# Performance work log

Hardware: AMD Instinct MI355X
Metric: run time of the kernel (lower is better)

Reference implementation:

```python
import jax, jax.numpy as jnp
import numpy as np

PZ = 8            # pz half-patch in get_dist_base
P = 2 * PZ        # patch side = 16
C, T, HF, WF = 128, 3, 256, 256
N = 2048          # number of keypoint pairs


def setup_inputs() -> dict:
    key = jax.random.key(0)
    ks = jax.random.split(key, 9)
    response = jax.random.normal(ks[0], (C, T, HF, WF), dtype=jnp.float32)
    ys1 = jax.random.randint(ks[1], (N,), 0, HF - P, dtype=jnp.int32)
    xs1 = jax.random.randint(ks[2], (N,), 0, WF - P, dtype=jnp.int32)
    ts1 = jax.random.randint(ks[3], (N,), 0, T, dtype=jnp.int32)
    ys2 = jax.random.randint(ks[4], (N,), 0, HF - P, dtype=jnp.int32)
    xs2 = jax.random.randint(ks[5], (N,), 0, WF - P, dtype=jnp.int32)
    ts2 = jax.random.randint(ks[6], (N,), 0, T, dtype=jnp.int32)
    pair_type = jax.random.randint(ks[7], (N,), 0, 3, dtype=jnp.int32)  # 0=BG,1=I,2=IS
    powers = 1.0 + jax.random.uniform(ks[8], (3,), dtype=jnp.float32)   # per-type exponent in [1,2)
    plus = jnp.ones((1,), dtype=jnp.float32)
    return dict(response=response, ys1=ys1, xs1=xs1, ts1=ts1,
                ys2=ys2, xs2=xs2, ts2=ts2, pair_type=pair_type,
                powers=powers, plus=plus)


def _gather_patches(response, ts, ys, xs):
    # response: [C, T, Hf, Wf] -> patches [N, C, P, P]
    c = response.shape[0]
    def one(t, y, x):
        return jax.lax.dynamic_slice(response, (0, t, y, x), (c, 1, P, P))[:, 0]
    return jax.vmap(one)(ts, ys, xs)


def _minmax_norm(p):
    # normalize_tensor: min-max over whole patch; identity if max==min
    mn = p.min(axis=(1, 2, 3), keepdims=True)
    mx = p.max(axis=(1, 2, 3), keepdims=True)
    rng = mx - mn
    return jnp.where(rng != 0, (p - mn) / jnp.where(rng == 0, 1.0, rng), p)


def reference(response, ys1, xs1, ts1, ys2, xs2, ts2, pair_type, powers, plus):
    P1 = _minmax_norm(_gather_patches(response, ts1, ys1, xs1))
    P2 = _minmax_norm(_gather_patches(response, ts2, ys2, xs2))
    pw = powers[pair_type][:, None, None, None]            # per-pair exponent
    d = jnp.mean(jnp.abs(P1 - P2) ** pw, axis=(1, 2, 3))   # losscal core, [N]
    per = jnp.where(pair_type == 2, d, 1.0 / (1.0 + d))    # IS -> losscal_1, BG/I -> losscal_2
    per = per + jnp.where(pair_type == 0, 0.0, plus[0] * 0.5)  # + plus/2 for I and IS
    return jnp.mean(per)                                   # lossbase / act
```

## Files before the change

### kernel.cpp

```cpp
#include <hip/hip_runtime.h>
#include <math.h>

#define CC 128
#define TT 3
#define HFD 256
#define WFD 256
#define PP 16
#define NPAIR 2048
#define HW (HFD * WFD)
#define POS (TT * HW)
#define CH_STRIDE POS
#define PATCH_ELEMS (CC * PP * PP)
#define BLOCK 256
#define TP 256

typedef float floatx2 __attribute__((ext_vector_type(2)));
typedef float floatx4 __attribute__((ext_vector_type(4)));

__global__ __launch_bounds__(BLOCK) void transpose_minmax_kernel(
    const float* __restrict__ resp,
    unsigned int* __restrict__ rt32,
    float* __restrict__ cmn, float* __restrict__ cmx) {
    __shared__ unsigned int tile32[TP][33];
    __shared__ float smn[4][TP], smx[4][TP];

    int p0 = blockIdx.x * TP;
    int pc = threadIdx.x & 63;
    int ph = threadIdx.x >> 6;

    const float* bp = resp + p0 + 4 * pc;

    float mn0 = INFINITY, mn1 = INFINITY, mn2 = INFINITY, mn3 = INFINITY;
    float mx0 = -INFINITY, mx1 = -INFINITY, mx2 = -INFINITY, mx3 = -INFINITY;

    #pragma unroll
    for (int k = 0; k < 8; ++k) {
        int q = k * 4 + ph;
        floatx4 l0 = *(const floatx4*)(bp + (size_t)(4 * q + 0) * CH_STRIDE);
        floatx4 l1 = *(const floatx4*)(bp + (size_t)(4 * q + 1) * CH_STRIDE);
        floatx4 l2 = *(const floatx4*)(bp + (size_t)(4 * q + 2) * CH_STRIDE);
        floatx4 l3 = *(const floatx4*)(bp + (size_t)(4 * q + 3) * CH_STRIDE);
        #pragma unroll
        for (int j = 0; j < 4; ++j) {
            float v0 = l0[j], v1 = l1[j], v2 = l2[j], v3 = l3[j];
            float mnj = fminf(fminf(v0, v1), fminf(v2, v3));
            float mxj = fmaxf(fmaxf(v0, v1), fmaxf(v2, v3));
            if (j == 0) { mn0 = fminf(mn0, mnj); mx0 = fmaxf(mx0, mxj); }
            if (j == 1) { mn1 = fminf(mn1, mnj); mx1 = fmaxf(mx1, mxj); }
            if (j == 2) { mn2 = fminf(mn2, mnj); mx2 = fmaxf(mx2, mxj); }
            if (j == 3) { mn3 = fminf(mn3, mnj); mx3 = fmaxf(mx3, mxj); }
            int w = __builtin_amdgcn_cvt_pk_fp8_f32(v0, v1, 0, false);
            w = __builtin_amdgcn_cvt_pk_fp8_f32(v2, v3, w, true);
            tile32[4 * pc + j][q] = (unsigned int)w;
        }
    }
    smn[ph][4 * pc + 0] = mn0; smx[ph][4 * pc + 0] = mx0;
    smn[ph][4 * pc + 1] = mn1; smx[ph][4 * pc + 1] = mx1;
    smn[ph][4 * pc + 2] = mn2; smx[ph][4 * pc + 2] = mx2;
    smn[ph][4 * pc + 3] = mn3; smx[ph][4 * pc + 3] = mx3;
    __syncthreads();

    int tp = threadIdx.x;
    cmn[p0 + tp] = fminf(fminf(smn[0][tp], smn[1][tp]), fminf(smn[2][tp], smn[3][tp]));
    cmx[p0 + tp] = fmaxf(fmaxf(smx[0][tp], smx[1][tp]), fmaxf(smx[2][tp], smx[3][tp]));

    #pragma unroll
    for (int j = 0; j < 32; ++j) {
        int u   = j * BLOCK + threadIdx.x;
        int pos = u >> 5;
        int c4  = u & 31;
        rt32[(((size_t)(p0 + pos)) << 5) + c4] = tile32[pos][c4];
    }
}

__device__ inline float pw_term(float va, float vb, float sc1, float nsc2, float K, float pw) {
    float d = fmaf(va, sc1, fmaf(vb, nsc2, K));
    return __builtin_amdgcn_exp2f(pw * __builtin_amdgcn_logf(fabsf(d)));
}

__device__ inline float quad_acc(unsigned int wa, unsigned int wb,
                                 float sc1, float nsc2, float K, float pw) {
    floatx2 a0 = __builtin_amdgcn_cvt_pk_f32_fp8((int)wa, false);
    floatx2 a1 = __builtin_amdgcn_cvt_pk_f32_fp8((int)wa, true);
    floatx2 b0 = __builtin_amdgcn_cvt_pk_f32_fp8((int)wb, false);
    floatx2 b1 = __builtin_amdgcn_cvt_pk_f32_fp8((int)wb, true);
    return pw_term(a0.x, b0.x, sc1, nsc2, K, pw) + pw_term(a0.y, b0.y, sc1, nsc2, K, pw)
         + pw_term(a1.x, b1.x, sc1, nsc2, K, pw) + pw_term(a1.y, b1.y, sc1, nsc2, K, pw);
}

__global__ __launch_bounds__(BLOCK) void pair_loss_kernel(
    const uint4* __restrict__ rt,
    const int* __restrict__ ts1, const int* __restrict__ ys1, const int* __restrict__ xs1,
    const int* __restrict__ ts2, const int* __restrict__ ys2, const int* __restrict__ xs2,
    const int* __restrict__ pair_type,
    const float* __restrict__ powers,
    const float* __restrict__ plus,
    const float* __restrict__ cmn, const float* __restrict__ cmx,
    float* __restrict__ per_out) {
    int i = blockIdx.x;
    int t1 = ts1[i], y1 = ys1[i], x1 = xs1[i];
    int t2 = ts2[i], y2 = ys2[i], x2 = xs2[i];
    int p1 = t1 * HW + y1 * WFD + x1;
    int p2 = t2 * HW + y2 * WFD + x2;

    int dy = threadIdx.x >> 4, dx = threadIdx.x & 15;
    int q1 = p1 + dy * WFD + dx;
    int q2 = p2 + dy * WFD + dx;
    float a0 = cmn[q1], a1 = cmx[q1];
    float b0 = cmn[q2], b1 = cmx[q2];
    #pragma unroll
    for (int off = 32; off > 0; off >>= 1) {
        a0 = fminf(a0, __shfl_down(a0, off));
        a1 = fmaxf(a1, __shfl_down(a1, off));
        b0 = fminf(b0, __shfl_down(b0, off));
        b1 = fmaxf(b1, __shfl_down(b1, off));
    }
    __shared__ float red[4][4];
    int wave = threadIdx.x >> 6;
    if ((threadIdx.x & 63) == 0) {
        red[wave][0] = a0; red[wave][1] = a1; red[wave][2] = b0; red[wave][3] = b1;
    }
    __syncthreads();
    float mn1 = fminf(fminf(red[0][0], red[1][0]), fminf(red[2][0], red[3][0]));
    float mx1 = fmaxf(fmaxf(red[0][1], red[1][1]), fmaxf(red[2][1], red[3][1]));
    float mn2 = fminf(fminf(red[0][2], red[1][2]), fminf(red[2][2], red[3][2]));
    float mx2 = fmaxf(fmaxf(red[0][3], red[1][3]), fmaxf(red[2][3], red[3][3]));

    float rg1 = mx1 - mn1, rg2 = mx2 - mn2;
    float sc1 = (rg1 != 0.0f) ? (1.0f / rg1) : 1.0f;
    float sh1 = (rg1 != 0.0f) ? mn1 : 0.0f;
    float sc2 = (rg2 != 0.0f) ? (1.0f / rg2) : 1.0f;
    float sh2 = (rg2 != 0.0f) ? mn2 : 0.0f;
    float nsc2 = -sc2;
    float K = sh2 * sc2 - sh1 * sc1;

    int   ptype = pair_type[i];
    float pw    = powers[ptype];

    int c16 = threadIdx.x & 7;
    int pdx = (threadIdx.x >> 3) & 15;
    int dyb = threadIdx.x >> 7;
    const uint4* A = rt + (((size_t)(p1 + pdx)) << 3) + c16;
    const uint4* B = rt + (((size_t)(p2 + pdx)) << 3) + c16;
    const size_t RSTR = (size_t)WFD << 3;

    float acc = 0.0f;
    #pragma unroll
    for (int j = 0; j < 8; ++j) {
        size_t off = (size_t)(dyb + 2 * j) * RSTR;
        uint4 wa = A[off];
        uint4 wb = B[off];
        acc += quad_acc(wa.x, wb.x, sc1, nsc2, K, pw);
        acc += quad_acc(wa.y, wb.y, sc1, nsc2, K, pw);
        acc += quad_acc(wa.z, wb.z, sc1, nsc2, K, pw);
        acc += quad_acc(wa.w, wb.w, sc1, nsc2, K, pw);
    }
    for (int off = 32; off > 0; off >>= 1) acc += __shfl_down(acc, off);
    __shared__ float ssum[BLOCK / 64];
    if ((threadIdx.x & 63) == 0) ssum[wave] = acc;
    __syncthreads();
    if (threadIdx.x == 0) {
        float total = ssum[0] + ssum[1] + ssum[2] + ssum[3];
        float dmean = total * (1.0f / (float)PATCH_ELEMS);
        float per = (ptype == 2) ? dmean : (1.0f / (1.0f + dmean));
        per += (ptype == 0) ? 0.0f : plus[0] * 0.5f;
        per_out[i] = per;
    }
}

__global__ __launch_bounds__(BLOCK) void final_mean_kernel(
    const float* __restrict__ per_out, float* __restrict__ out) {
    float acc = 0.0f;
    for (int i = threadIdx.x; i < NPAIR; i += BLOCK) acc += per_out[i];
    for (int off = 32; off > 0; off >>= 1) acc += __shfl_down(acc, off);
    __shared__ float ssum[BLOCK / 64];
    int wave = threadIdx.x >> 6;
    if ((threadIdx.x & 63) == 0) ssum[wave] = acc;
    __syncthreads();
    if (threadIdx.x == 0) {
        float total = ssum[0] + ssum[1] + ssum[2] + ssum[3];
        out[0] = total * (1.0f / (float)NPAIR);
    }
}

extern "C" void kernel_launch(void* const* d_in, const int* in_sizes, int n_in,
                              void* d_out, int out_size, void* d_ws, size_t ws_size,
                              hipStream_t stream) {
    const float* resp      = (const float*)d_in[0];
    const int*   ys1       = (const int*)d_in[1];
    const int*   xs1       = (const int*)d_in[2];
    const int*   ts1       = (const int*)d_in[3];
    const int*   ys2       = (const int*)d_in[4];
    const int*   xs2       = (const int*)d_in[5];
    const int*   ts2       = (const int*)d_in[6];
    const int*   pair_type = (const int*)d_in[7];
    const float* powers    = (const float*)d_in[8];
    const float* plus      = (const float*)d_in[9];
    float*       out       = (float*)d_out;

    unsigned int* rt32 = (unsigned int*)d_ws;
    float* cmn     = (float*)(rt32 + (size_t)POS * 32);
    float* cmx     = cmn + POS;
    float* per_out = cmx + POS;

    transpose_minmax_kernel<<<POS / TP, BLOCK, 0, stream>>>(resp, rt32, cmn, cmx);

    pair_loss_kernel<<<NPAIR, BLOCK, 0, stream>>>(
        (const uint4*)rt32, ts1, ys1, xs1, ts2, ys2, xs2, pair_type, powers, plus,
        cmn, cmx, per_out);

    final_mean_kernel<<<1, BLOCK, 0, stream>>>(per_out, out);
}
```

Baseline: 192.6 us.

## Fuse final mean via atomics, prefetch patch loads, remap transpose thread layout

Removes the separate final-mean kernel: each pair block atomically adds its loss, and the last block, detected through an atomic counter, writes the mean. The accumulators are zeroed in the transpose kernel. The pair kernel issues its patch loads before the min/max reduction so that memory latency overlaps with the reduction. The transpose thread mapping is swapped so neighbouring lanes cover different channels, which changes the coalescing and LDS access patterns. Atomic float summation makes the result order nondeterministic.

```diff
diff --git a/kernel.cpp b/kernel.cpp
--- a/kernel.cpp
+++ b/kernel.cpp
@@ -20,13 +20,19 @@
 __global__ __launch_bounds__(BLOCK) void transpose_minmax_kernel(
     const float* __restrict__ resp,
     unsigned int* __restrict__ rt32,
-    float* __restrict__ cmn, float* __restrict__ cmx) {
+    float* __restrict__ cmn, float* __restrict__ cmx,
+    float* __restrict__ acc_ws, unsigned int* __restrict__ count_ws) {
     __shared__ unsigned int tile32[TP][33];
     __shared__ float smn[4][TP], smx[4][TP];
 
+    if (blockIdx.x == 0 && threadIdx.x == 0) {
+        acc_ws[0] = 0.0f;
+        count_ws[0] = 0u;
+    }
+
     int p0 = blockIdx.x * TP;
-    int pc = threadIdx.x & 63;
-    int ph = threadIdx.x >> 6;
+    int pc = threadIdx.x >> 2;
+    int ph = threadIdx.x & 3;
 
     const float* bp = resp + p0 + 4 * pc;
 
@@ -96,12 +102,28 @@
     const float* __restrict__ powers,
     const float* __restrict__ plus,
     const float* __restrict__ cmn, const float* __restrict__ cmx,
-    float* __restrict__ per_out) {
+    float* __restrict__ acc_ws, unsigned int* __restrict__ count_ws,
+    float* __restrict__ out) {
     int i = blockIdx.x;
     int t1 = ts1[i], y1 = ys1[i], x1 = xs1[i];
     int t2 = ts2[i], y2 = ys2[i], x2 = xs2[i];
     int p1 = t1 * HW + y1 * WFD + x1;
     int p2 = t2 * HW + y2 * WFD + x2;
+
+    int c16 = threadIdx.x & 7;
+    int pdx = (threadIdx.x >> 3) & 15;
+    int dyb = threadIdx.x >> 7;
+    const uint4* A = rt + (((size_t)(p1 + pdx)) << 3) + c16;
+    const uint4* B = rt + (((size_t)(p2 + pdx)) << 3) + c16;
+    const size_t RSTR = (size_t)WFD << 3;
+
+    uint4 wa[8], wb[8];
+    #pragma unroll
+    for (int j = 0; j < 8; ++j) {
+        size_t off = (size_t)(dyb + 2 * j) * RSTR;
+        wa[j] = A[off];
+        wb[j] = B[off];
+    }
 
     int dy = threadIdx.x >> 4, dx = threadIdx.x & 15;
     int q1 = p1 + dy * WFD + dx;
@@ -137,23 +159,13 @@
     int   ptype = pair_type[i];
     float pw    = powers[ptype];
 
-    int c16 = threadIdx.x & 7;
-    int pdx = (threadIdx.x >> 3) & 15;
-    int dyb = threadIdx.x >> 7;
-    const uint4* A = rt + (((size_t)(p1 + pdx)) << 3) + c16;
-    const uint4* B = rt + (((size_t)(p2 + pdx)) << 3) + c16;
-    const size_t RSTR = (size_t)WFD << 3;
-
     float acc = 0.0f;
     #pragma unroll
     for (int j = 0; j < 8; ++j) {
-        size_t off = (size_t)(dyb + 2 * j) * RSTR;
-        uint4 wa = A[off];
-        uint4 wb = B[off];
-        acc += quad_acc(wa.x, wb.x, sc1, nsc2, K, pw);
-        acc += quad_acc(wa.y, wb.y, sc1, nsc2, K, pw);
-        acc += quad_acc(wa.z, wb.z, sc1, nsc2, K, pw);
-        acc += quad_acc(wa.w, wb.w, sc1, nsc2, K, pw);
+        acc += quad_acc(wa[j].x, wb[j].x, sc1, nsc2, K, pw);
+        acc += quad_acc(wa[j].y, wb[j].y, sc1, nsc2, K, pw);
+        acc += quad_acc(wa[j].z, wb[j].z, sc1, nsc2, K, pw);
+        acc += quad_acc(wa[j].w, wb[j].w, sc1, nsc2, K, pw);
     }
     for (int off = 32; off > 0; off >>= 1) acc += __shfl_down(acc, off);
     __shared__ float ssum[BLOCK / 64];
@@ -164,22 +176,14 @@
         float dmean = total * (1.0f / (float)PATCH_ELEMS);
         float per = (ptype == 2) ? dmean : (1.0f / (1.0f + dmean));
         per += (ptype == 0) ? 0.0f : plus[0] * 0.5f;
-        per_out[i] = per;
-    }
-}
-
-__global__ __launch_bounds__(BLOCK) void final_mean_kernel(
-    const float* __restrict__ per_out, float* __restrict__ out) {
-    float acc = 0.0f;
-    for (int i = threadIdx.x; i < NPAIR; i += BLOCK) acc += per_out[i];
-    for (int off = 32; off > 0; off >>= 1) acc += __shfl_down(acc, off);
-    __shared__ float ssum[BLOCK / 64];
-    int wave = threadIdx.x >> 6;
-    if ((threadIdx.x & 63) == 0) ssum[wave] = acc;
-    __syncthreads();
-    if (threadIdx.x == 0) {
-        float total = ssum[0] + ssum[1] + ssum[2] + ssum[3];
-        out[0] = total * (1.0f / (float)NPAIR);
+        atomicAdd(acc_ws, per);
+        __threadfence();
+        unsigned int old = atomicAdd(count_ws, 1u);
+        if (old == NPAIR - 1) {
+            __threadfence();
+            float total_all = atomicAdd(acc_ws, 0.0f);
+            out[0] = total_all * (1.0f / (float)NPAIR);
+        }
     }
 }
 
@@ -199,15 +203,15 @@
     float*       out       = (float*)d_out;
 
     unsigned int* rt32 = (unsigned int*)d_ws;
-    float* cmn     = (float*)(rt32 + (size_t)POS * 32);
-    float* cmx     = cmn + POS;
-    float* per_out = cmx + POS;
-
-    transpose_minmax_kernel<<<POS / TP, BLOCK, 0, stream>>>(resp, rt32, cmn, cmx);
+    float* cmn            = (float*)(rt32 + (size_t)POS * 32);
+    float* cmx            = cmn + POS;
+    float* acc_ws         = cmx + POS;
+    unsigned int* count_ws = (unsigned int*)(acc_ws + 1);
+
+    transpose_minmax_kernel<<<POS / TP, BLOCK, 0, stream>>>(
+        resp, rt32, cmn, cmx, acc_ws, count_ws);
 
     pair_loss_kernel<<<NPAIR, BLOCK, 0, stream>>>(
         (const uint4*)rt32, ts1, ys1, xs1, ts2, ys2, xs2, pair_type, powers, plus,
-        cmn, cmx, per_out);
-
-    final_mean_kernel<<<1, BLOCK, 0, stream>>>(per_out, out);
-}
+        cmn, cmx, acc_ws, count_ws, out);
+}
```

Result: slower. 247.4 us (+28.4%).
